# Optimization experiments

Hardware: AMD Instinct MI355X
Metric: run time of the kernel (lower is better)

Reference implementation:

```python
import jax, jax.numpy as jnp
import numpy as np

T = 16384
D_IN = 512
D_HID = 512
D_OUT = 512


def setup_inputs() -> dict:
    key = jax.random.key(0)
    ks = jax.random.split(key, 7)
    s_in = 1.0 / np.sqrt(D_IN)
    s_hid = 1.0 / np.sqrt(D_HID)
    xs = jax.random.normal(ks[0], (T, D_IN), dtype=jnp.float32)
    Wz = jax.random.uniform(ks[1], (D_HID, D_IN), jnp.float32, -s_in, s_in)
    bz = jax.random.uniform(ks[2], (D_HID,), jnp.float32, -s_in, s_in)
    Wh = jax.random.uniform(ks[3], (D_HID, D_IN), jnp.float32, -s_in, s_in)
    bh = jax.random.uniform(ks[4], (D_HID,), jnp.float32, -s_in, s_in)
    Wo = jax.random.uniform(ks[5], (D_OUT, D_HID), jnp.float32, -s_hid, s_hid)
    bo = jax.random.uniform(ks[6], (D_OUT,), jnp.float32, -s_hid, s_hid)
    return {"xs": xs, "Wz": Wz, "bz": bz, "Wh": Wh, "bh": bh, "Wo": Wo, "bo": bo}


def _combine(first, second):
    a0, b0 = first
    a1, b1 = second
    return (a0 * a1, a1 * b0 + b1)


def reference(xs, Wz, bz, Wh, bh, Wo, bo):
    # gates and candidate hidden states: [T, H]
    zs = jax.nn.sigmoid(xs @ Wz.T + bz)
    hs = xs @ Wh.T + bh
    # prepend identity element (a=1, b=0) for the h_0 = 0 initial state
    a = jnp.concatenate([jnp.ones((1, zs.shape[1]), zs.dtype), 1.0 - zs], axis=0)
    b = jnp.concatenate([jnp.zeros((1, zs.shape[1]), zs.dtype), zs * hs], axis=0)
    _, states = jax.lax.associative_scan(_combine, (a, b))  # [T+1, H]
    return states[1:] @ Wo.T + bo  # [T, D_OUT]
```

## Files before the change

kernel.cpp:

```cpp
#include <hip/hip_runtime.h>
#include <hip/hip_bf16.h>
#include <cstdint>
#include <cmath>

#define T_SEQ 16384
#define DMODEL 512
#define NCHUNK 512
#define LCHUNK 32
#define W_N    (DMODEL * DMODEL)
#define N4_W   (W_N / 4)
#define N4_W3  (3 * N4_W)

typedef __bf16 bf16x8 __attribute__((ext_vector_type(8)));
typedef float  f32x4  __attribute__((ext_vector_type(4)));

using bf16 = __hip_bfloat16;

__device__ __forceinline__ void load_lds16(const void* g, void* l) {
    __builtin_amdgcn_global_load_lds((const __attribute__((address_space(1))) void*)g,
                                     (__attribute__((address_space(3))) void*)l,
                                     16, 0, 0);
}

__device__ __forceinline__ unsigned short f2bf(float f) {
    union { float f; unsigned u; } v; v.f = f;
    const unsigned r = (v.u + 0x7FFFu + ((v.u >> 16) & 1u)) >> 16;
    return (unsigned short)r;
}
__device__ __forceinline__ float bf2f(unsigned short u) {
    union { unsigned u; float f; } v; v.u = ((unsigned)u) << 16;
    return v.f;
}

__device__ __forceinline__ void comb(float& A, float& B, float fA, float fB,
                                     float sA, float sB) {
    A = fA * sA;
    B = sA * fB + sB;
}

__global__ __launch_bounds__(256) void k_convert_w(
    const float* __restrict__ Wz, const float* __restrict__ Wh,
    const float* __restrict__ Wo,
    bf16* __restrict__ Wz_c, bf16* __restrict__ Wh_c, bf16* __restrict__ Wo_c)
{
    const int i = blockIdx.x * 256 + threadIdx.x;
    if (i >= N4_W3) return;
    const int w = i >> 16;
    const int o = i & 65535;
    const float* src = (w == 0) ? Wz : (w == 1) ? Wh : Wo;
    bf16* dst = (w == 0) ? Wz_c : (w == 1) ? Wh_c : Wo_c;
    const float4 v = ((const float4*)src)[o];
    ushort4 r;
    r.x = f2bf(v.x); r.y = f2bf(v.y); r.z = f2bf(v.z); r.w = f2bf(v.w);
    ((ushort4*)dst)[o] = r;
}

__global__ __launch_bounds__(256, 2) void gemm_zh(
    const float* __restrict__ xs, const bf16* __restrict__ Wz, const float* __restrict__ bz,
    const bf16* __restrict__ Wh, const float* __restrict__ bh,
    unsigned int* __restrict__ ab_ws,
    float* __restrict__ AaggT, float* __restrict__ BaggT)
{
    __shared__ __bf16 As[128 * 64];
    __shared__ __bf16 Zs[128 * 64];
    __shared__ __bf16 Hs[128 * 64];

    const int tid  = threadIdx.x;
    const int bm   = blockIdx.x;
    const int bn   = blockIdx.y;
    const int lane = tid & 63;
    const int wave = tid >> 6;
    const int wm   = wave >> 1;
    const int wn   = wave & 1;

    f32x4 accz[4][4], acch[4][4];
    #pragma unroll
    for (int i = 0; i < 4; ++i)
        #pragma unroll
        for (int j = 0; j < 4; ++j) {
            accz[i][j] = (f32x4){0.f, 0.f, 0.f, 0.f};
            acch[i][j] = (f32x4){0.f, 0.f, 0.f, 0.f};
        }

    const int row0 = tid >> 3;
    const int k8   = tid & 7;
    const bf16* zg = Wz + (size_t)(bn * 128) * DMODEL + k8 * 8;
    const bf16* hg = Wh + (size_t)(bn * 128) * DMODEL + k8 * 8;

    const int frow = tid >> 4;
    const int f4   = tid & 15;
    const float* xg = xs + ((size_t)(bm * 128) + frow) * DMODEL + f4 * 4;

    const int quad = lane >> 4;
    const int col  = lane & 15;

    for (int k0 = 0; k0 < DMODEL; k0 += 64) {
        #pragma unroll
        for (int it = 0; it < 4; ++it) {
            const int row   = row0 + it * 32;
            const int chunk = it * 256 + tid;
            load_lds16(zg + (size_t)row * DMODEL + k0, &Zs[chunk * 8]);
            load_lds16(hg + (size_t)row * DMODEL + k0, &Hs[chunk * 8]);
        }
        #pragma unroll
        for (int it2 = 0; it2 < 8; ++it2) {
            const int row = frow + it2 * 16;
            const float4 v = *(const float4*)(xg + (size_t)(it2 * 16) * DMODEL + k0);
            __hip_bfloat162 p0 = __float22bfloat162_rn(make_float2(v.x, v.y));
            __hip_bfloat162 p1 = __float22bfloat162_rn(make_float2(v.z, v.w));
            uint2 pk;
            pk.x = *(const unsigned*)&p0;
            pk.y = *(const unsigned*)&p1;
            *(uint2*)&As[row * 64 + f4 * 4] = pk;
        }
        __syncthreads();

        #pragma unroll
        for (int kk = 0; kk < 2; ++kk) {
            const int kb = kk * 32 + quad * 8;
            bf16x8 af[4], zf[4], hf[4];
            #pragma unroll
            for (int i = 0; i < 4; ++i) {
                const int am  = wm * 64 + i * 16 + col;
                const int bnr = wn * 64 + i * 16 + col;
                af[i] = *(const bf16x8*)&As[am * 64 + kb];
                zf[i] = *(const bf16x8*)&Zs[bnr * 64 + kb];
                hf[i] = *(const bf16x8*)&Hs[bnr * 64 + kb];
            }
            #pragma unroll
            for (int i = 0; i < 4; ++i)
                #pragma unroll
                for (int j = 0; j < 4; ++j) {
                    accz[i][j] = __builtin_amdgcn_mfma_f32_16x16x32_bf16(af[i], zf[j], accz[i][j], 0, 0, 0);
                    acch[i][j] = __builtin_amdgcn_mfma_f32_16x16x32_bf16(af[i], hf[j], acch[i][j], 0, 0, 0);
                }
        }
        __syncthreads();
    }

    const int c_lo = bm * 4 + wm * 2;
    #pragma unroll
    for (int j = 0; j < 4; ++j) {
        const int n = bn * 128 + wn * 64 + j * 16 + col;
        const float bzv = bz[n];
        const float bhv = bh[n];
        float cA[4], cB[4];
        #pragma unroll
        for (int i = 0; i < 4; ++i) {
            const int mbase = bm * 128 + wm * 64 + i * 16 + quad * 4;
            float A = 1.f, B = 0.f;
            #pragma unroll
            for (int r = 0; r < 4; ++r) {
                const float zpre = accz[i][j][r] + bzv;
                const float hpre = acch[i][j][r] + bhv;
                const float z = 1.f / (1.f + __expf(-zpre));
                const float a = 1.f - z;
                const float b = z * hpre;
                const size_t idx = (size_t)(mbase + r) * DMODEL + n;
                ab_ws[idx] = (unsigned)f2bf(a) | ((unsigned)f2bf(b) << 16);
                A = a * A;
                B = a * B + b;
            }
            cA[i] = A; cB[i] = B;
        }
        #pragma unroll
        for (int i = 0; i < 4; ++i) {
            float pA = __shfl_xor(cA[i], 16);
            float pB = __shfl_xor(cB[i], 16);
            const bool hi1 = quad & 1;
            comb(cA[i], cB[i], hi1 ? pA : cA[i], hi1 ? pB : cB[i],
                               hi1 ? cA[i] : pA, hi1 ? cB[i] : pB);
            pA = __shfl_xor(cA[i], 32);
            pB = __shfl_xor(cB[i], 32);
            const bool hi2 = quad >> 1;
            comb(cA[i], cB[i], hi2 ? pA : cA[i], hi2 ? pB : cB[i],
                               hi2 ? cA[i] : pA, hi2 ? cB[i] : pB);
        }
        float Alo, Blo, Ahi, Bhi;
        comb(Alo, Blo, cA[0], cB[0], cA[1], cB[1]);
        comb(Ahi, Bhi, cA[2], cB[2], cA[3], cB[3]);
        if (quad == 0) {
            AaggT[(size_t)n * NCHUNK + c_lo]     = Alo;
            BaggT[(size_t)n * NCHUNK + c_lo]     = Blo;
            AaggT[(size_t)n * NCHUNK + c_lo + 1] = Ahi;
            BaggT[(size_t)n * NCHUNK + c_lo + 1] = Bhi;
        }
    }
}

__global__ __launch_bounds__(512) void scan_p2(
    const float* __restrict__ AaggT, const float* __restrict__ BaggT,
    float* __restrict__ HpreT)
{
    const int h = blockIdx.x;
    const int c = threadIdx.x;
    __shared__ float sA[NCHUNK], sB[NCHUNK];

    float A = AaggT[(size_t)h * NCHUNK + c];
    float B = BaggT[(size_t)h * NCHUNK + c];
    sA[c] = A; sB[c] = B;
    __syncthreads();

    for (int off = 1; off < NCHUNK; off <<= 1) {
        float pA = 1.f, pB = 0.f;
        if (c >= off) { pA = sA[c - off]; pB = sB[c - off]; }
        __syncthreads();
        const float nB = A * pB + B;
        const float nA = A * pA;
        A = nA; B = nB;
        sA[c] = A; sB[c] = B;
        __syncthreads();
    }
    const float hp = (c == 0) ? 0.f : sB[c - 1];
    HpreT[(size_t)h * NCHUNK + c] = hp;
}

__global__ __launch_bounds__(256) void scan_p3(
    const unsigned int* __restrict__ ab_ws, const float* __restrict__ HpreT,
    unsigned short* __restrict__ states)
{
    const int tid = threadIdx.x;
    const int c   = blockIdx.x;
    float H0 = HpreT[(size_t)(2 * tid) * NCHUNK + c];
    float H1 = HpreT[(size_t)(2 * tid + 1) * NCHUNK + c];
    const size_t rowbase = (size_t)(c * LCHUNK) * DMODEL;
    #pragma unroll 8
    for (int i = 0; i < LCHUNK; ++i) {
        const size_t row = rowbase + (size_t)i * DMODEL;
        const uint2 u = ((const uint2*)(ab_ws + row))[tid];
        const float a0 = bf2f((unsigned short)(u.x & 0xFFFFu));
        const float b0 = bf2f((unsigned short)(u.x >> 16));
        const float a1 = bf2f((unsigned short)(u.y & 0xFFFFu));
        const float b1 = bf2f((unsigned short)(u.y >> 16));
        H0 = a0 * H0 + b0;
        H1 = a1 * H1 + b1;
        ushort2 s; s.x = f2bf(H0); s.y = f2bf(H1);
        ((ushort2*)(states + row))[tid] = s;
    }
}

__global__ __launch_bounds__(256, 2) void gemm_out(
    const bf16* __restrict__ states, const bf16* __restrict__ Wo, const float* __restrict__ bo,
    float* __restrict__ out)
{
    __shared__ __bf16 As[128 * 64];
    __shared__ __bf16 Bs[128 * 64];

    const int tid  = threadIdx.x;
    const int bm   = blockIdx.x;
    const int bn   = blockIdx.y;
    const int lane = tid & 63;
    const int wave = tid >> 6;
    const int wm   = wave >> 1;
    const int wn   = wave & 1;

    f32x4 acc[4][4];
    #pragma unroll
    for (int i = 0; i < 4; ++i)
        #pragma unroll
        for (int j = 0; j < 4; ++j)
            acc[i][j] = (f32x4){0.f, 0.f, 0.f, 0.f};

    const int row0 = tid >> 3;
    const int k8   = tid & 7;

    const bf16* ag = states + (size_t)(bm * 128) * DMODEL + k8 * 8;
    const bf16* bg = Wo     + (size_t)(bn * 128) * DMODEL + k8 * 8;

    const int quad = lane >> 4;
    const int col  = lane & 15;

    for (int k0 = 0; k0 < DMODEL; k0 += 64) {
        #pragma unroll
        for (int it = 0; it < 4; ++it) {
            const int row   = row0 + it * 32;
            const int chunk = it * 256 + tid;
            load_lds16(ag + (size_t)row * DMODEL + k0, &As[chunk * 8]);
            load_lds16(bg + (size_t)row * DMODEL + k0, &Bs[chunk * 8]);
        }
        __syncthreads();

        #pragma unroll
        for (int kk = 0; kk < 2; ++kk) {
            const int kb = kk * 32 + quad * 8;
            bf16x8 af[4], bf[4];
            #pragma unroll
            for (int i = 0; i < 4; ++i) {
                af[i] = *(const bf16x8*)&As[(wm * 64 + i * 16 + col) * 64 + kb];
                bf[i] = *(const bf16x8*)&Bs[(wn * 64 + i * 16 + col) * 64 + kb];
            }
            #pragma unroll
            for (int i = 0; i < 4; ++i)
                #pragma unroll
                for (int j = 0; j < 4; ++j)
                    acc[i][j] = __builtin_amdgcn_mfma_f32_16x16x32_bf16(af[i], bf[j], acc[i][j], 0, 0, 0);
        }
        __syncthreads();
    }

    #pragma unroll
    for (int j = 0; j < 4; ++j) {
        const int n = bn * 128 + wn * 64 + j * 16 + col;
        const float bov = bo[n];
        #pragma unroll
        for (int i = 0; i < 4; ++i) {
            const int mbase = bm * 128 + wm * 64 + i * 16 + quad * 4;
            #pragma unroll
            for (int r = 0; r < 4; ++r)
                out[(size_t)(mbase + r) * DMODEL + n] = acc[i][j][r] + bov;
        }
    }
}

extern "C" void kernel_launch(void* const* d_in, const int* in_sizes, int n_in,
                              void* d_out, int out_size, void* d_ws, size_t ws_size,
                              hipStream_t stream)
{
    const float* xs = (const float*)d_in[0];
    const float* Wz = (const float*)d_in[1];
    const float* bz = (const float*)d_in[2];
    const float* Wh = (const float*)d_in[3];
    const float* bh = (const float*)d_in[4];
    const float* Wo = (const float*)d_in[5];
    const float* bo = (const float*)d_in[6];
    float* out = (float*)d_out;

    char* w = (char*)d_ws;
    bf16*  Wz_c   = (bf16*) (w);
    bf16*  Wh_c   = (bf16*) (w + 524288ull);
    bf16*  Wo_c   = (bf16*) (w + 1048576ull);
    unsigned int*   ab_ws  = (unsigned int*)  (w + 1572864ull);
    unsigned short* states = (unsigned short*)(w + 35127296ull);
    float* AaggT  = (float*)(w + 51904512ull);
    float* BaggT  = (float*)(w + 52953088ull);
    float* HpreT  = (float*)(w + 54001664ull);

    k_convert_w<<<(N4_W3 + 255) / 256, 256, 0, stream>>>(Wz, Wh, Wo, Wz_c, Wh_c, Wo_c);
    gemm_zh<<<dim3(128, 4), 256, 0, stream>>>(xs, Wz_c, bz, Wh_c, bh, ab_ws, AaggT, BaggT);
    scan_p2<<<DMODEL, NCHUNK, 0, stream>>>(AaggT, BaggT, HpreT);
    scan_p3<<<NCHUNK, 256, 0, stream>>>(ab_ws, HpreT, states);
    gemm_out<<<dim3(128, 4), 256, 0, stream>>>((const bf16*)states, Wo_c, bo, out);
}
```

Measured before the change: 152.3 us.

## Double-buffer GEMM LDS tiles with XOR swizzle and split scan_p3 across channels

Both GEMM kernels now use BK=32 double-buffered LDS tiles: the next tile's global-to-LDS loads (and register-staged x loads) are issued before computing the current tile, with a single barrier per step. An XOR swizzle is applied to LDS row layout for both writes and fragment reads to reduce bank conflicts. scan_p3 is split into two blocks per chunk, each thread handling one channel, doubling parallelism at the cost of narrower memory accesses. The smaller K step means more loop iterations and barriers, in exchange for overlap of memory and MFMA work.

```diff
diff --git a/kernel.cpp b/kernel.cpp
--- a/kernel.cpp
+++ b/kernel.cpp
@@ -10,6 +10,8 @@
 #define W_N    (DMODEL * DMODEL)
 #define N4_W   (W_N / 4)
 #define N4_W3  (3 * N4_W)
+#define BK     32
+#define NT     (DMODEL / BK)
 
 typedef __bf16 bf16x8 __attribute__((ext_vector_type(8)));
 typedef float  f32x4  __attribute__((ext_vector_type(4)));
@@ -61,9 +63,9 @@
     unsigned int* __restrict__ ab_ws,
     float* __restrict__ AaggT, float* __restrict__ BaggT)
 {
-    __shared__ __bf16 As[128 * 64];
-    __shared__ __bf16 Zs[128 * 64];
-    __shared__ __bf16 Hs[128 * 64];
+    __shared__ __bf16 As[2][128 * BK];
+    __shared__ __bf16 Zs[2][128 * BK];
+    __shared__ __bf16 Hs[2][128 * BK];
 
     const int tid  = threadIdx.x;
     const int bm   = blockIdx.x;
@@ -72,6 +74,8 @@
     const int wave = tid >> 6;
     const int wm   = wave >> 1;
     const int wn   = wave & 1;
+    const int quad = lane >> 4;
+    const int col  = lane & 15;
 
     f32x4 accz[4][4], acch[4][4];
     #pragma unroll
@@ -82,61 +86,80 @@
             acch[i][j] = (f32x4){0.f, 0.f, 0.f, 0.f};
         }
 
-    const int row0 = tid >> 3;
-    const int k8   = tid & 7;
-    const bf16* zg = Wz + (size_t)(bn * 128) * DMODEL + k8 * 8;
-    const bf16* hg = Wh + (size_t)(bn * 128) * DMODEL + k8 * 8;
-
-    const int frow = tid >> 4;
-    const int f4   = tid & 15;
+    const int wrow = tid >> 2;
+    const int wq   = (tid & 3) ^ ((tid >> 3) & 3);
+    const bf16* zg = Wz + (size_t)(bn * 128 + wrow) * DMODEL + wq * 8;
+    const bf16* hg = Wh + (size_t)(bn * 128 + wrow) * DMODEL + wq * 8;
+
+    const int frow = tid >> 3;
+    const int f4   = tid & 7;
     const float* xg = xs + ((size_t)(bm * 128) + frow) * DMODEL + f4 * 4;
-
-    const int quad = lane >> 4;
-    const int col  = lane & 15;
-
-    for (int k0 = 0; k0 < DMODEL; k0 += 64) {
+    const int xoff = frow * BK + ((((f4 >> 1) ^ ((frow >> 1) & 3))) << 3) + (f4 & 1) * 4;
+
+    const int fq = quad ^ ((col >> 1) & 3);
+    int offA[4], offB[4];
+    #pragma unroll
+    for (int i = 0; i < 4; ++i) {
+        offA[i] = (wm * 64 + i * 16 + col) * BK + fq * 8;
+        offB[i] = (wn * 64 + i * 16 + col) * BK + fq * 8;
+    }
+
+    float4 xr[4];
+
+    auto XLOAD = [&](int t) {
+        const int k0 = t * BK;
+        #pragma unroll
+        for (int it = 0; it < 4; ++it)
+            xr[it] = *(const float4*)(xg + (size_t)(it * 32) * DMODEL + k0);
+    };
+    auto STAGE_W = [&](int t, int p) {
+        const int k0 = t * BK;
+        #pragma unroll
+        for (int it = 0; it < 2; ++it) {
+            const int chunk = it * 256 + tid;
+            load_lds16(zg + (size_t)(it * 64) * DMODEL + k0, &Zs[p][chunk * 8]);
+            load_lds16(hg + (size_t)(it * 64) * DMODEL + k0, &Hs[p][chunk * 8]);
+        }
+    };
+    auto XWRITE = [&](int p) {
         #pragma unroll
         for (int it = 0; it < 4; ++it) {
-            const int row   = row0 + it * 32;
-            const int chunk = it * 256 + tid;
-            load_lds16(zg + (size_t)row * DMODEL + k0, &Zs[chunk * 8]);
-            load_lds16(hg + (size_t)row * DMODEL + k0, &Hs[chunk * 8]);
-        }
-        #pragma unroll
-        for (int it2 = 0; it2 < 8; ++it2) {
-            const int row = frow + it2 * 16;
-            const float4 v = *(const float4*)(xg + (size_t)(it2 * 16) * DMODEL + k0);
-            __hip_bfloat162 p0 = __float22bfloat162_rn(make_float2(v.x, v.y));
-            __hip_bfloat162 p1 = __float22bfloat162_rn(make_float2(v.z, v.w));
+            __hip_bfloat162 p0 = __float22bfloat162_rn(make_float2(xr[it].x, xr[it].y));
+            __hip_bfloat162 p1 = __float22bfloat162_rn(make_float2(xr[it].z, xr[it].w));
             uint2 pk;
             pk.x = *(const unsigned*)&p0;
             pk.y = *(const unsigned*)&p1;
-            *(uint2*)&As[row * 64 + f4 * 4] = pk;
-        }
+            *(uint2*)&As[p][xoff + it * 32 * BK] = pk;
+        }
+    };
+    auto COMPUTE = [&](int p) {
+        bf16x8 af[4], zf[4], hf[4];
+        #pragma unroll
+        for (int i = 0; i < 4; ++i) {
+            af[i] = *(const bf16x8*)&As[p][offA[i]];
+            zf[i] = *(const bf16x8*)&Zs[p][offB[i]];
+            hf[i] = *(const bf16x8*)&Hs[p][offB[i]];
+        }
+        #pragma unroll
+        for (int i = 0; i < 4; ++i)
+            #pragma unroll
+            for (int j = 0; j < 4; ++j) {
+                accz[i][j] = __builtin_amdgcn_mfma_f32_16x16x32_bf16(af[i], zf[j], accz[i][j], 0, 0, 0);
+                acch[i][j] = __builtin_amdgcn_mfma_f32_16x16x32_bf16(af[i], hf[j], acch[i][j], 0, 0, 0);
+            }
+    };
+
+    XLOAD(0); STAGE_W(0, 0); XWRITE(0);
+    __syncthreads();
+    for (int t = 0; t < NT - 1; ++t) {
+        const int p = t & 1;
+        XLOAD(t + 1);
+        STAGE_W(t + 1, p ^ 1);
+        COMPUTE(p);
+        XWRITE(p ^ 1);
         __syncthreads();
-
-        #pragma unroll
-        for (int kk = 0; kk < 2; ++kk) {
-            const int kb = kk * 32 + quad * 8;
-            bf16x8 af[4], zf[4], hf[4];
-            #pragma unroll
-            for (int i = 0; i < 4; ++i) {
-                const int am  = wm * 64 + i * 16 + col;
-                const int bnr = wn * 64 + i * 16 + col;
-                af[i] = *(const bf16x8*)&As[am * 64 + kb];
-                zf[i] = *(const bf16x8*)&Zs[bnr * 64 + kb];
-                hf[i] = *(const bf16x8*)&Hs[bnr * 64 + kb];
-            }
-            #pragma unroll
-            for (int i = 0; i < 4; ++i)
-                #pragma unroll
-                for (int j = 0; j < 4; ++j) {
-                    accz[i][j] = __builtin_amdgcn_mfma_f32_16x16x32_bf16(af[i], zf[j], accz[i][j], 0, 0, 0);
-                    acch[i][j] = __builtin_amdgcn_mfma_f32_16x16x32_bf16(af[i], hf[j], acch[i][j], 0, 0, 0);
-                }
-        }
-        __syncthreads();
-    }
+    }
+    COMPUTE((NT - 1) & 1);
 
     const int c_lo = bm * 4 + wm * 2;
     #pragma unroll
@@ -221,21 +244,16 @@
 {
     const int tid = threadIdx.x;
     const int c   = blockIdx.x;
-    float H0 = HpreT[(size_t)(2 * tid) * NCHUNK + c];
-    float H1 = HpreT[(size_t)(2 * tid + 1) * NCHUNK + c];
-    const size_t rowbase = (size_t)(c * LCHUNK) * DMODEL;
+    const int ch  = blockIdx.y * 256 + tid;
+    float H = HpreT[(size_t)ch * NCHUNK + c];
+    const size_t base = (size_t)(c * LCHUNK) * DMODEL + ch;
     #pragma unroll 8
     for (int i = 0; i < LCHUNK; ++i) {
-        const size_t row = rowbase + (size_t)i * DMODEL;
-        const uint2 u = ((const uint2*)(ab_ws + row))[tid];
-        const float a0 = bf2f((unsigned short)(u.x & 0xFFFFu));
-        const float b0 = bf2f((unsigned short)(u.x >> 16));
-        const float a1 = bf2f((unsigned short)(u.y & 0xFFFFu));
-        const float b1 = bf2f((unsigned short)(u.y >> 16));
-        H0 = a0 * H0 + b0;
-        H1 = a1 * H1 + b1;
-        ushort2 s; s.x = f2bf(H0); s.y = f2bf(H1);
-        ((ushort2*)(states + row))[tid] = s;
+        const unsigned u = ab_ws[base + (size_t)i * DMODEL];
+        const float a = bf2f((unsigned short)(u & 0xFFFFu));
+        const float b = bf2f((unsigned short)(u >> 16));
+        H = a * H + b;
+        states[base + (size_t)i * DMODEL] = f2bf(H);
     }
 }
 
@@ -243,8 +261,8 @@
     const bf16* __restrict__ states, const bf16* __restrict__ Wo, const float* __restrict__ bo,
     float* __restrict__ out)
 {
-    __shared__ __bf16 As[128 * 64];
-    __shared__ __bf16 Bs[128 * 64];
+    __shared__ __bf16 As[2][128 * BK];
+    __shared__ __bf16 Bs[2][128 * BK];
 
     const int tid  = threadIdx.x;
     const int bm   = blockIdx.x;
@@ -253,6 +271,8 @@
     const int wave = tid >> 6;
     const int wm   = wave >> 1;
     const int wn   = wave & 1;
+    const int quad = lane >> 4;
+    const int col  = lane & 15;
 
     f32x4 acc[4][4];
     #pragma unroll
@@ -261,42 +281,51 @@
         for (int j = 0; j < 4; ++j)
             acc[i][j] = (f32x4){0.f, 0.f, 0.f, 0.f};
 
-    const int row0 = tid >> 3;
-    const int k8   = tid & 7;
-
-    const bf16* ag = states + (size_t)(bm * 128) * DMODEL + k8 * 8;
-    const bf16* bg = Wo     + (size_t)(bn * 128) * DMODEL + k8 * 8;
-
-    const int quad = lane >> 4;
-    const int col  = lane & 15;
-
-    for (int k0 = 0; k0 < DMODEL; k0 += 64) {
-        #pragma unroll
-        for (int it = 0; it < 4; ++it) {
-            const int row   = row0 + it * 32;
+    const int wrow = tid >> 2;
+    const int wq   = (tid & 3) ^ ((tid >> 3) & 3);
+    const bf16* ag = states + (size_t)(bm * 128 + wrow) * DMODEL + wq * 8;
+    const bf16* bg = Wo     + (size_t)(bn * 128 + wrow) * DMODEL + wq * 8;
+
+    const int fq = quad ^ ((col >> 1) & 3);
+    int offA[4], offB[4];
+    #pragma unroll
+    for (int i = 0; i < 4; ++i) {
+        offA[i] = (wm * 64 + i * 16 + col) * BK + fq * 8;
+        offB[i] = (wn * 64 + i * 16 + col) * BK + fq * 8;
+    }
+
+    auto STAGE = [&](int t, int p) {
+        const int k0 = t * BK;
+        #pragma unroll
+        for (int it = 0; it < 2; ++it) {
             const int chunk = it * 256 + tid;
-            load_lds16(ag + (size_t)row * DMODEL + k0, &As[chunk * 8]);
-            load_lds16(bg + (size_t)row * DMODEL + k0, &Bs[chunk * 8]);
-        }
+            load_lds16(ag + (size_t)(it * 64) * DMODEL + k0, &As[p][chunk * 8]);
+            load_lds16(bg + (size_t)(it * 64) * DMODEL + k0, &Bs[p][chunk * 8]);
+        }
+    };
+    auto COMPUTE = [&](int p) {
+        bf16x8 af[4], bf[4];
+        #pragma unroll
+        for (int i = 0; i < 4; ++i) {
+            af[i] = *(const bf16x8*)&As[p][offA[i]];
+            bf[i] = *(const bf16x8*)&Bs[p][offB[i]];
+        }
+        #pragma unroll
+        for (int i = 0; i < 4; ++i)
+            #pragma unroll
+            for (int j = 0; j < 4; ++j)
+                acc[i][j] = __builtin_amdgcn_mfma_f32_16x16x32_bf16(af[i], bf[j], acc[i][j], 0, 0, 0);
+    };
+
+    STAGE(0, 0);
+    __syncthreads();
+    for (int t = 0; t < NT - 1; ++t) {
+        const int p = t & 1;
+        STAGE(t + 1, p ^ 1);
+        COMPUTE(p);
         __syncthreads();
-
-        #pragma unroll
-        for (int kk = 0; kk < 2; ++kk) {
-            const int kb = kk * 32 + quad * 8;
-            bf16x8 af[4], bf[4];
-            #pragma unroll
-            for (int i = 0; i < 4; ++i) {
-                af[i] = *(const bf16x8*)&As[(wm * 64 + i * 16 + col) * 64 + kb];
-                bf[i] = *(const bf16x8*)&Bs[(wn * 64 + i * 16 + col) * 64 + kb];
-            }
-            #pragma unroll
-            for (int i = 0; i < 4; ++i)
-                #pragma unroll
-                for (int j = 0; j < 4; ++j)
-                    acc[i][j] = __builtin_amdgcn_mfma_f32_16x16x32_bf16(af[i], bf[j], acc[i][j], 0, 0, 0);
-        }
-        __syncthreads();
-    }
+    }
+    COMPUTE((NT - 1) & 1);
 
     #pragma unroll
     for (int j = 0; j < 4; ++j) {
@@ -338,6 +367,6 @@
     k_convert_w<<<(N4_W3 + 255) / 256, 256, 0, stream>>>(Wz, Wh, Wo, Wz_c, Wh_c, Wo_c);
     gemm_zh<<<dim3(128, 4), 256, 0, stream>>>(xs, Wz_c, bz, Wh_c, bh, ab_ws, AaggT, BaggT);
     scan_p2<<<DMODEL, NCHUNK, 0, stream>>>(AaggT, BaggT, HpreT);
-    scan_p3<<<NCHUNK, 256, 0, stream>>>(ab_ws, HpreT, states);
+    scan_p3<<<dim3(NCHUNK, 2), 256, 0, stream>>>(ab_ws, HpreT, states);
     gemm_out<<<dim3(128, 4), 256, 0, stream>>>((const bf16*)states, Wo_c, bo, out);
 }
```

After: 167.4 us. 1.1x slower.
